# Performance work log

Measured on AMD Instinct MI355X. Metric: run time of the kernel, lower is better.

## Reference

```python
import jax, jax.numpy as jnp
import numpy as np

B = 64            # batch of graphs
E = 8978          # edge-simplices per graph (nodes of the Hodge-1 graph)
E2 = E // 2       # after Graclus pair-pooling
K = 4             # Laguerre polynomial order
DEG = 16          # avg degree of the (edge-)adjacency
SLOPE = 0.33      # LeakyReLU negative slope
EPS = 1e-5        # BatchNorm eps


def _make_edges(rng, b, n, deg):
    # block-diagonal batched edge list: each graph only connects within itself
    offs = np.repeat(np.arange(b, dtype=np.int64) * n, n * deg)
    dst = np.tile(np.repeat(np.arange(n, dtype=np.int64), deg), b) + offs
    src = rng.integers(0, n, size=b * n * deg) + offs
    return np.stack([src, dst]).astype(np.int32)


def setup_inputs() -> dict:
    rng = np.random.default_rng(0)
    ks = jax.random.split(jax.random.key(0), 12)
    N1 = B * E
    ei1 = _make_edges(rng, B, E, DEG)
    ei2 = _make_edges(rng, B, E2, DEG)
    return {
        "x_s": jax.random.normal(ks[0], (N1, 1), jnp.float32),
        "edge_index_s": jnp.asarray(ei1),
        "edge_weight_s": jax.random.uniform(ks[1], (ei1.shape[1],), jnp.float32) * (2.0 / DEG),
        "edge_index_s1": jnp.asarray(ei2),
        "edge_weight_s1": jax.random.uniform(ks[2], (ei2.shape[1],), jnp.float32) * (2.0 / DEG),
        "W0": jax.random.normal(ks[3], (K, 1, 32), jnp.float32) * 0.3,
        "b0": jnp.zeros((32,), jnp.float32),
        "g0": jnp.ones((32,), jnp.float32),
        "be0": jnp.zeros((32,), jnp.float32),
        "W1": jax.random.normal(ks[4], (K, 32, 32), jnp.float32) * 0.1,
        "b1": jnp.zeros((32,), jnp.float32),
        "g1": jnp.ones((32,), jnp.float32),
        "be1": jnp.zeros((32,), jnp.float32),
        "W2": jax.random.normal(ks[5], (K, 32, 1), jnp.float32) * 0.1,
        "b2": jnp.zeros((1,), jnp.float32),
        "g2": jnp.ones((1,), jnp.float32),
        "be2": jnp.zeros((1,), jnp.float32),
        "lin1_W": jax.random.normal(ks[6], (E2, 256), jnp.float32) * 0.02,
        "lin1_b": jnp.zeros((256,), jnp.float32),
        "bn1_g": jnp.ones((256,), jnp.float32),
        "bn1_b": jnp.zeros((256,), jnp.float32),
        "lin2_W": jax.random.normal(ks[7], (256, 128), jnp.float32) * 0.06,
        "lin2_b": jnp.zeros((128,), jnp.float32),
        "bn2_g": jnp.ones((128,), jnp.float32),
        "bn2_b": jnp.zeros((128,), jnp.float32),
        "lin3_W": jax.random.normal(ks[8], (128, 1), jnp.float32) * 0.09,
        "lin3_b": jnp.zeros((1,), jnp.float32),
    }


def _laguerre_layer(x, src, dst, ew, W, b, gamma, beta, n):
    """HodgeLaguerreConv (K-order Laguerre recurrence over sparse L) + BatchNorm + LeakyReLU."""
    def matvec(v):  # (L v)[i] = sum_j w_ij v[j]
        return jax.ops.segment_sum(ew[:, None] * v[src], dst, num_segments=n)
    Tp = x                      # L_0(L) x = x
    out = Tp @ W[0]
    Tc = x - matvec(x)          # L_1(L) x = x - L x
    out = out + Tc @ W[1]
    for k in range(1, K - 1):   # L_{k+1} = ((2k+1-L) L_k - k L_{k-1}) / (k+1)
        Tn = ((2 * k + 1) * Tc - matvec(Tc) - k * Tp) / (k + 1)
        out = out + Tn @ W[k + 1]
        Tp, Tc = Tc, Tn
    out = out + b
    out = gamma * (out - out.mean(0)) * jax.lax.rsqrt(out.var(0) + EPS) + beta
    return jnp.where(out > 0, out, SLOPE * out)


def _bn(h, g, b):
    return g * (h - h.mean(0)) * jax.lax.rsqrt(h.var(0) + EPS) + b


def reference(x_s, edge_index_s, edge_weight_s, edge_index_s1, edge_weight_s1,
              W0, b0, g0, be0, W1, b1, g1, be1, W2, b2, g2, be2,
              lin1_W, lin1_b, bn1_g, bn1_b, lin2_W, lin2_b, bn2_g, bn2_b,
              lin3_W, lin3_b):
    N1, N2 = B * E, B * E2
    x = _laguerre_layer(x_s, edge_index_s[0], edge_index_s[1], edge_weight_s,
                        W0, b0, g0, be0, N1)
    # Graclus pooling: merge matched node pairs by max over features
    x = x.reshape(B, E2, 2, x.shape[-1]).max(axis=2).reshape(N2, -1)
    x = _laguerre_layer(x, edge_index_s1[0], edge_index_s1[1], edge_weight_s1,
                        W1, b1, g1, be1, N2)
    x = _laguerre_layer(x, edge_index_s1[0], edge_index_s1[1], edge_weight_s1,
                        W2, b2, g2, be2, N2)
    x = x.reshape(B, E2)        # last conv has 1 channel
    h = jax.nn.relu(_bn(x @ lin1_W + lin1_b, bn1_g, bn1_b))
    h = jax.nn.relu(_bn(h @ lin2_W + lin2_b, bn2_g, bn2_b))
    return h @ lin3_W + lin3_b  # [B, num_classes=1]
```

## Files before the change

### kernel.cpp

```cpp
#include <hip/hip_runtime.h>
#include <cstdint>

#define SLOPE 0.33f

static constexpr int B_   = 64;
static constexpr int E1_  = 8978;
static constexpr int E2_  = 4489;
static constexpr int N1_  = B_ * E1_;
static constexpr int N2_  = B_ * E2_;
static constexpr int DEG_ = 16;
static constexpr int QTR_ = 2245;
static constexpr int QTR2_ = 1123;
static constexpr int MVGRID = (N2_ * 32) / 256;
static constexpr int PROJ_GRID = (N2_ + 511) / 512;
static constexpr double EPS_ = 1e-5;

__device__ __forceinline__ float lrelu(float v) { return v > 0.f ? v : SLOPE * v; }
__device__ __forceinline__ float dot4(float4 a, float4 b) {
  return a.x * b.x + a.y * b.y + a.z * b.z + a.w * b.w;
}

__global__ __launch_bounds__(256) void k0_mv1(const float* __restrict__ x,
    const int* __restrict__ src, const float* __restrict__ ew, float* __restrict__ T1) {
  __shared__ float sx[E1_];
  int g = blockIdx.x >> 2, q = blockIdx.x & 3;
  int gbase = g * E1_;
  for (int j = threadIdx.x; j < E1_; j += 256) sx[j] = x[gbase + j];
  __syncthreads();
  int start = q * QTR_, end = min(start + QTR_, E1_);
  for (int i = start + (int)threadIdx.x; i < end; i += 256) {
    int node = gbase + i;
    const int4* s4 = (const int4*)(src + (size_t)node * DEG_);
    const float4* w4 = (const float4*)(ew + (size_t)node * DEG_);
    float acc = 0.f;
#pragma unroll
    for (int j = 0; j < 4; ++j) {
      int4 s = s4[j]; float4 w = w4[j];
      acc += w.x * sx[s.x - gbase] + w.y * sx[s.y - gbase]
           + w.z * sx[s.z - gbase] + w.w * sx[s.w - gbase];
    }
    T1[node] = sx[i] - acc;
  }
}

__global__ __launch_bounds__(256) void k0_mv2(const float* __restrict__ x,
    const int* __restrict__ src, const float* __restrict__ ew,
    const float* __restrict__ T1, float* __restrict__ T2) {
  __shared__ float sT[E1_];
  int g = blockIdx.x >> 2, q = blockIdx.x & 3;
  int gbase = g * E1_;
  for (int j = threadIdx.x; j < E1_; j += 256) sT[j] = T1[gbase + j];
  __syncthreads();
  int start = q * QTR_, end = min(start + QTR_, E1_);
  for (int i = start + (int)threadIdx.x; i < end; i += 256) {
    int node = gbase + i;
    const int4* s4 = (const int4*)(src + (size_t)node * DEG_);
    const float4* w4 = (const float4*)(ew + (size_t)node * DEG_);
    float acc = 0.f;
#pragma unroll
    for (int j = 0; j < 4; ++j) {
      int4 s = s4[j]; float4 w = w4[j];
      acc += w.x * sT[s.x - gbase] + w.y * sT[s.y - gbase]
           + w.z * sT[s.z - gbase] + w.w * sT[s.w - gbase];
    }
    T2[node] = (3.f * sT[i] - acc - x[node]) * 0.5f;
  }
}

__global__ __launch_bounds__(256) void k0_mv3(const float* __restrict__ x,
    const int* __restrict__ src, const float* __restrict__ ew,
    const float* __restrict__ T1, const float* __restrict__ T2,
    float* __restrict__ T3, double* mom) {
  __shared__ float sT[E1_];
  __shared__ double sred[4 * 14];
  int g = blockIdx.x >> 2, q = blockIdx.x & 3;
  int gbase = g * E1_;
  for (int j = threadIdx.x; j < E1_; j += 256) sT[j] = T2[gbase + j];
  __syncthreads();
  double m[14];
#pragma unroll
  for (int j = 0; j < 14; ++j) m[j] = 0.0;
  int start = q * QTR_, end = min(start + QTR_, E1_);
  for (int i = start + (int)threadIdx.x; i < end; i += 256) {
    int node = gbase + i;
    const int4* s4 = (const int4*)(src + (size_t)node * DEG_);
    const float4* w4 = (const float4*)(ew + (size_t)node * DEG_);
    float acc = 0.f;
#pragma unroll
    for (int j = 0; j < 4; ++j) {
      int4 s = s4[j]; float4 w = w4[j];
      acc += w.x * sT[s.x - gbase] + w.y * sT[s.y - gbase]
           + w.z * sT[s.z - gbase] + w.w * sT[s.w - gbase];
    }
    float t1 = T1[node];
    float t2 = sT[i];
    float t3 = (5.f * t2 - acc - 2.f * t1) * (1.f / 3.f);
    T3[node] = t3;
    double d0 = x[node], d1 = t1, d2 = t2, d3 = t3;
    m[0] += d0; m[1] += d1; m[2] += d2; m[3] += d3;
    m[4] += d0 * d0; m[5] += d0 * d1; m[6] += d0 * d2; m[7] += d0 * d3;
    m[8] += d1 * d1; m[9] += d1 * d2; m[10] += d1 * d3;
    m[11] += d2 * d2; m[12] += d2 * d3; m[13] += d3 * d3;
  }
  int lane = threadIdx.x & 63, wid = threadIdx.x >> 6;
#pragma unroll
  for (int j = 0; j < 14; ++j) {
    double v = m[j];
    for (int o = 32; o; o >>= 1) v += __shfl_down(v, o);
    if (lane == 0) sred[wid * 14 + j] = v;
  }
  __syncthreads();
  if (threadIdx.x < 14) {
    double s = sred[threadIdx.x] + sred[14 + threadIdx.x] + sred[28 + threadIdx.x] + sred[42 + threadIdx.x];
    atomicAdd(&mom[threadIdx.x], s);
  }
}

__global__ void k0_params(const double* __restrict__ mom, const float* __restrict__ W0,
    const float* __restrict__ g0, const float* __restrict__ be0,
    float* __restrict__ scale0, float* __restrict__ shiftE0) {
  int c = threadIdx.x;
  if (c >= 32) return;
  double inv = 1.0 / (double)N1_;
  double mm[4];
#pragma unroll
  for (int k = 0; k < 4; ++k) mm[k] = mom[k] * inv;
  double M[4][4];
  M[0][0] = mom[4] * inv;  M[0][1] = mom[5] * inv;  M[0][2] = mom[6] * inv;  M[0][3] = mom[7] * inv;
  M[1][1] = mom[8] * inv;  M[1][2] = mom[9] * inv;  M[1][3] = mom[10] * inv;
  M[2][2] = mom[11] * inv; M[2][3] = mom[12] * inv; M[3][3] = mom[13] * inv;
  M[1][0] = M[0][1]; M[2][0] = M[0][2]; M[3][0] = M[0][3];
  M[2][1] = M[1][2]; M[3][1] = M[1][3]; M[3][2] = M[2][3];
  double w[4];
#pragma unroll
  for (int k = 0; k < 4; ++k) w[k] = W0[k * 32 + c];
  double mean = 0.0;
#pragma unroll
  for (int k = 0; k < 4; ++k) mean += w[k] * mm[k];
  double e2 = 0.0;
#pragma unroll
  for (int k = 0; k < 4; ++k)
#pragma unroll
    for (int l = 0; l < 4; ++l) e2 += M[k][l] * w[k] * w[l];
  double var = e2 - mean * mean;
  double sc = (double)g0[c] / sqrt(var + EPS_);
  scale0[c] = (float)sc;
  shiftE0[c] = (float)((double)be0[c] - sc * mean);
}

__global__ __launch_bounds__(256) void k0_pool(const float* __restrict__ x,
    const float* __restrict__ T1, const float* __restrict__ T2, const float* __restrict__ T3,
    const float* __restrict__ W0, const float* __restrict__ scale0,
    const float* __restrict__ shiftE0, float* __restrict__ x1) {
  int gid = blockIdx.x * 256 + threadIdx.x;
  int grp = gid >> 5, c = gid & 31;
  if (grp >= N2_) return;
  int b = grp / E2_, j = grp - b * E2_;
  int ga = b * E1_ + 2 * j, gb = ga + 1;
  float w0 = W0[c], w1 = W0[32 + c], w2 = W0[64 + c], w3 = W0[96 + c];
  float da = x[ga] * w0 + T1[ga] * w1 + T2[ga] * w2 + T3[ga] * w3;
  float db = x[gb] * w0 + T1[gb] * w1 + T2[gb] * w2 + T3[gb] * w3;
  float sc = scale0[c], sh = shiftE0[c];
  float ya = lrelu(sc * da + sh), yb = lrelu(sc * db + sh);
  x1[grp * 32 + c] = fmaxf(ya, yb);
}

__global__ __launch_bounds__(256) void k1_projall(const float* __restrict__ X,
    const float* __restrict__ W1, float4* __restrict__ P4) {
  __shared__ float4 Wl[128 * 8];
  const float4 cfs[4] = { {0.f, 0.f, 0.f, -1.f / 6.f},
                          {0.f, 0.f, 0.5f, 1.5f},
                          {0.f, -1.f, -2.f, -3.f},
                          {1.f, 1.f, 1.f, 1.f} };
  for (int e = threadIdx.x; e < 1024; e += 256) {
    int o = e >> 3, qq = e & 7;
    int j = o >> 5, cp = o & 31;
    float4 cf = cfs[j];
    float4 w;
    {
      const float* wp = W1 + (4 * qq + 0) * 32 + cp;
      w.x = cf.x * wp[0] + cf.y * wp[1024] + cf.z * wp[2048] + cf.w * wp[3072];
    }
    {
      const float* wp = W1 + (4 * qq + 1) * 32 + cp;
      w.y = cf.x * wp[0] + cf.y * wp[1024] + cf.z * wp[2048] + cf.w * wp[3072];
    }
    {
      const float* wp = W1 + (4 * qq + 2) * 32 + cp;
      w.z = cf.x * wp[0] + cf.y * wp[1024] + cf.z * wp[2048] + cf.w * wp[3072];
    }
    {
      const float* wp = W1 + (4 * qq + 3) * 32 + cp;
      w.w = cf.x * wp[0] + cf.y * wp[1024] + cf.z * wp[2048] + cf.w * wp[3072];
    }
    Wl[e] = w;
  }
  __syncthreads();
  int rA = blockIdx.x * 512 + threadIdx.x;
  int rB = rA + 256;
  bool okA = rA < N2_, okB = rB < N2_;
  if (!okA) return;
  float4 xA[8], xB[8];
  {
    const float4* pa = (const float4*)(X + (size_t)rA * 32);
#pragma unroll
    for (int t = 0; t < 8; ++t) xA[t] = pa[t];
  }
  if (okB) {
    const float4* pb = (const float4*)(X + (size_t)rB * 32);
#pragma unroll
    for (int t = 0; t < 8; ++t) xB[t] = pb[t];
  } else {
#pragma unroll
    for (int t = 0; t < 8; ++t) xB[t] = {0.f, 0.f, 0.f, 0.f};
  }
  for (int oq = 0; oq < 32; ++oq) {
    float4 aA = {0.f, 0.f, 0.f, 0.f}, aB = {0.f, 0.f, 0.f, 0.f};
    const float4* wr = Wl + oq * 32;
#pragma unroll
    for (int qq = 0; qq < 8; ++qq) {
      float4 w0 = wr[0 * 8 + qq];
      float4 w1 = wr[1 * 8 + qq];
      float4 w2 = wr[2 * 8 + qq];
      float4 w3 = wr[3 * 8 + qq];
      float4 xa = xA[qq], xb = xB[qq];
      aA.x += dot4(xa, w0); aA.y += dot4(xa, w1); aA.z += dot4(xa, w2); aA.w += dot4(xa, w3);
      aB.x += dot4(xb, w0); aB.y += dot4(xb, w1); aB.z += dot4(xb, w2); aB.w += dot4(xb, w3);
    }
    P4[(size_t)oq * N2_ + rA] = aA;
    if (okB) P4[(size_t)oq * N2_ + rB] = aB;
  }
}

__global__ __launch_bounds__(1024) void k1_chain(const float4* __restrict__ P4,
    float4* __restrict__ O4, const int* __restrict__ src,
    const float* __restrict__ ew, double* st) {
  __shared__ float4 bA[E2_], bB[E2_];
  __shared__ float sacc[8];
  int v = (blockIdx.x & 7) * 64 + (blockIdx.x >> 3);
  int g = v >> 3, cg = v & 7;
  int gbase = g * E2_;
  int tid = threadIdx.x;
  if (tid < 8) sacc[tid] = 0.f;
  {
    const float4* sp = P4 + (size_t)cg * N2_ + gbase;
    for (int i = tid; i < E2_; i += 1024) bA[i] = sp[i];
  }
  float4* cur = bA;
  float4* nxt = bB;
  for (int s = 1; s <= 3; ++s) {
    __syncthreads();
    const float4* selfp = P4 + (size_t)(s * 8 + cg) * N2_ + gbase;
    for (int n = tid; n < E2_; n += 1024) {
      const int4* s4 = (const int4*)(src + (size_t)(gbase + n) * DEG_);
      const float4* w4 = (const float4*)(ew + (size_t)(gbase + n) * DEG_);
      float4 acc = selfp[n];
#pragma unroll
      for (int j = 0; j < 4; ++j) {
        int4 sx = s4[j]; float4 w = w4[j];
        float4 g0 = cur[sx.x - gbase];
        float4 g1 = cur[sx.y - gbase];
        float4 g2 = cur[sx.z - gbase];
        float4 g3 = cur[sx.w - gbase];
        acc.x += w.x * g0.x + w.y * g1.x + w.z * g2.x + w.w * g3.x;
        acc.y += w.x * g0.y + w.y * g1.y + w.z * g2.y + w.w * g3.y;
        acc.z += w.x * g0.z + w.y * g1.z + w.z * g2.z + w.w * g3.z;
        acc.w += w.x * g0.w + w.y * g1.w + w.z * g2.w + w.w * g3.w;
      }
      nxt[n] = acc;
    }
    float4* t = cur; cur = nxt; nxt = t;
  }
  __syncthreads();
  float4* op = O4 + (size_t)cg * N2_ + gbase;
  float4 s1 = {0.f, 0.f, 0.f, 0.f}, s2 = {0.f, 0.f, 0.f, 0.f};
  for (int n = tid; n < E2_; n += 1024) {
    float4 vv = cur[n];
    op[n] = vv;
    s1.x += vv.x; s1.y += vv.y; s1.z += vv.z; s1.w += vv.w;
    s2.x += vv.x * vv.x; s2.y += vv.y * vv.y; s2.z += vv.z * vv.z; s2.w += vv.w * vv.w;
  }
  for (int o = 32; o; o >>= 1) {
    s1.x += __shfl_down(s1.x, o); s1.y += __shfl_down(s1.y, o);
    s1.z += __shfl_down(s1.z, o); s1.w += __shfl_down(s1.w, o);
    s2.x += __shfl_down(s2.x, o); s2.y += __shfl_down(s2.y, o);
    s2.z += __shfl_down(s2.z, o); s2.w += __shfl_down(s2.w, o);
  }
  if ((tid & 63) == 0) {
    atomicAdd(&sacc[0], s1.x); atomicAdd(&sacc[1], s1.y);
    atomicAdd(&sacc[2], s1.z); atomicAdd(&sacc[3], s1.w);
    atomicAdd(&sacc[4], s2.x); atomicAdd(&sacc[5], s2.y);
    atomicAdd(&sacc[6], s2.z); atomicAdd(&sacc[7], s2.w);
  }
  __syncthreads();
  if (tid < 4) {
    int ch = cg * 4 + tid;
    atomicAdd(&st[ch], (double)sacc[tid]);
    atomicAdd(&st[32 + ch], (double)sacc[4 + tid]);
  }
}

__global__ void k1_params(const double* __restrict__ sum, const double* __restrict__ sq,
    const float* __restrict__ g1, const float* __restrict__ be1,
    float* __restrict__ scale1, float* __restrict__ shiftE1) {
  int c = threadIdx.x;
  if (c >= 32) return;
  double mean = sum[c] / (double)N2_;
  double var = sq[c] / (double)N2_ - mean * mean;
  double sc = (double)g1[c] / sqrt(var + EPS_);
  scale1[c] = (float)sc;
  shiftE1[c] = (float)((double)be1[c] - sc * mean);
}

__global__ __launch_bounds__(256) void k2_proj(const float* __restrict__ X,
    const float* __restrict__ W2, const float* __restrict__ scale1,
    const float* __restrict__ shiftE1,
    float* __restrict__ u0, float* __restrict__ u1,
    float* __restrict__ u2, float* __restrict__ u3) {
  __shared__ float qv[4][32];
  __shared__ float fsc[32], fsh[32];
  int tid = threadIdx.x;
  if (tid < 128) {
    int cp = tid & 31, j = tid >> 5;
    float w0 = W2[cp], w1 = W2[32 + cp], w2 = W2[64 + cp], w3 = W2[96 + cp];
    float q;
    if (j == 0)      q = w0 + w1 + w2 + w3;
    else if (j == 1) q = -w1 - 2.f * w2 - 3.f * w3;
    else if (j == 2) q = 0.5f * w2 + 1.5f * w3;
    else             q = -w3 * (1.f / 6.f);
    qv[j][cp] = q;
  }
  if (tid < 32) { fsc[tid] = scale1[tid]; fsh[tid] = shiftE1[tid]; }
  __syncthreads();
  int node = blockIdx.x * 256 + tid;
  if (node >= N2_) return;
  const float4* xf = (const float4*)X;
  float a0 = 0.f, a1 = 0.f, a2 = 0.f, a3 = 0.f;
#pragma unroll
  for (int t = 0; t < 8; ++t) {
    float4 v = xf[(size_t)t * N2_ + node];
    float f0 = lrelu(fsc[4 * t] * v.x + fsh[4 * t]);
    float f1 = lrelu(fsc[4 * t + 1] * v.y + fsh[4 * t + 1]);
    float f2_ = lrelu(fsc[4 * t + 2] * v.z + fsh[4 * t + 2]);
    float f3 = lrelu(fsc[4 * t + 3] * v.w + fsh[4 * t + 3]);
    a0 += f0 * qv[0][4 * t] + f1 * qv[0][4 * t + 1] + f2_ * qv[0][4 * t + 2] + f3 * qv[0][4 * t + 3];
    a1 += f0 * qv[1][4 * t] + f1 * qv[1][4 * t + 1] + f2_ * qv[1][4 * t + 2] + f3 * qv[1][4 * t + 3];
    a2 += f0 * qv[2][4 * t] + f1 * qv[2][4 * t + 1] + f2_ * qv[2][4 * t + 2] + f3 * qv[2][4 * t + 3];
    a3 += f0 * qv[3][4 * t] + f1 * qv[3][4 * t + 1] + f2_ * qv[3][4 * t + 2] + f3 * qv[3][4 * t + 3];
  }
  u0[node] = a0; u1[node] = a1; u2[node] = a2; u3[node] = a3;
}

__global__ __launch_bounds__(256) void k2_step(const float* __restrict__ z,
    const int* __restrict__ src, const float* __restrict__ ew,
    const float* __restrict__ u, float* __restrict__ zo,
    int do_stats, double* st2) {
  __shared__ float sz[E2_];
  __shared__ double sred[4][2];
  int g = blockIdx.x >> 2, q = blockIdx.x & 3;
  int gbase = g * E2_;
  for (int j = threadIdx.x; j < E2_; j += 256) sz[j] = z[gbase + j];
  __syncthreads();
  int start = q * QTR2_, end = min(start + QTR2_, E2_);
  double aS = 0.0, aQ = 0.0;
  for (int i = start + (int)threadIdx.x; i < end; i += 256) {
    int node = gbase + i;
    const int4* s4 = (const int4*)(src + (size_t)node * DEG_);
    const float4* w4 = (const float4*)(ew + (size_t)node * DEG_);
    float acc = 0.f;
#pragma unroll
    for (int j = 0; j < 4; ++j) {
      int4 s = s4[j]; float4 w = w4[j];
      acc += w.x * sz[s.x - gbase] + w.y * sz[s.y - gbase]
           + w.z * sz[s.z - gbase] + w.w * sz[s.w - gbase];
    }
    float val = u[node] + acc;
    zo[node] = val;
    if (do_stats) { aS += val; aQ += (double)val * (double)val; }
  }
  if (do_stats) {
    int lane = threadIdx.x & 63, wid = threadIdx.x >> 6;
    for (int o = 32; o; o >>= 1) { aS += __shfl_down(aS, o); aQ += __shfl_down(aQ, o); }
    if (lane == 0) { sred[wid][0] = aS; sred[wid][1] = aQ; }
    __syncthreads();
    if (threadIdx.x == 0) {
      double s = sred[0][0] + sred[1][0] + sred[2][0] + sred[3][0];
      double qq = sred[0][1] + sred[1][1] + sred[2][1] + sred[3][1];
      atomicAdd(&st2[0], s); atomicAdd(&st2[1], qq);
    }
  }
}

__global__ void k2_params(const double* __restrict__ st2, const float* __restrict__ g2,
    const float* __restrict__ be2, float* __restrict__ p ) {
  if (threadIdx.x != 0) return;
  double mean = st2[0] / (double)N2_;
  double var = st2[1] / (double)N2_ - mean * mean;
  double sc = (double)g2[0] / sqrt(var + EPS_);
  p[128] = (float)sc;
  p[129] = (float)((double)be2[0] - sc * mean);
}

__global__ __launch_bounds__(256) void k3_gemm1(const float* __restrict__ out2,
    const float* __restrict__ lin1W, const float* __restrict__ p, float* h1pre) {
  __shared__ float f2v[4][284];
  float sc = p[128], sh = p[129];
  int bs = blockIdx.x & 15, rs = blockIdx.x >> 4;
  int b0 = bs * 4;
  int r0 = rs * 281;
  int nr = min(281, E2_ - r0);
  int c = threadIdx.x;
#pragma unroll
  for (int b = 0; b < 4; ++b)
    for (int j = c; j < 284; j += 256)
      f2v[b][j] = (j < nr) ? lrelu(sc * out2[(b0 + b) * E2_ + r0 + j] + sh) : 0.f;
  __syncthreads();
  float acc0 = 0.f, acc1 = 0.f, acc2 = 0.f, acc3 = 0.f;
  int nr4 = nr & ~3;
  int j = 0;
  for (; j < nr4; j += 4) {
    const float* wp = lin1W + (size_t)(r0 + j) * 256 + c;
    float w0 = wp[0], w1 = wp[256], w2 = wp[512], w3 = wp[768];
    float4 f0 = *(const float4*)&f2v[0][j];
    float4 f1 = *(const float4*)&f2v[1][j];
    float4 f2_ = *(const float4*)&f2v[2][j];
    float4 f3 = *(const float4*)&f2v[3][j];
    acc0 += f0.x * w0 + f0.y * w1 + f0.z * w2 + f0.w * w3;
    acc1 += f1.x * w0 + f1.y * w1 + f1.z * w2 + f1.w * w3;
    acc2 += f2_.x * w0 + f2_.y * w1 + f2_.z * w2 + f2_.w * w3;
    acc3 += f3.x * w0 + f3.y * w1 + f3.z * w2 + f3.w * w3;
  }
  for (; j < nr; ++j) {
    float w = lin1W[(size_t)(r0 + j) * 256 + c];
    acc0 += f2v[0][j] * w;
    acc1 += f2v[1][j] * w;
    acc2 += f2v[2][j] * w;
    acc3 += f2v[3][j] * w;
  }
  atomicAdd(&h1pre[(b0 + 0) * 256 + c], acc0);
  atomicAdd(&h1pre[(b0 + 1) * 256 + c], acc1);
  atomicAdd(&h1pre[(b0 + 2) * 256 + c], acc2);
  atomicAdd(&h1pre[(b0 + 3) * 256 + c], acc3);
}

__global__ __launch_bounds__(256) void k4_bn1(const float* __restrict__ h1pre,
    const float* __restrict__ g, const float* __restrict__ be, float* __restrict__ h1) {
  int c = threadIdx.x;
  float vs[64];
  double s = 0.0, q = 0.0;
  for (int b = 0; b < 64; ++b) { float v = h1pre[b * 256 + c]; vs[b] = v; s += v; q += (double)v * v; }
  double mean = s / 64.0, var = q / 64.0 - mean * mean;
  double scd = (double)g[c] / sqrt(var + EPS_);
  double shd = (double)be[c] - scd * mean;
  for (int b = 0; b < 64; ++b) {
    float y = (float)(scd * vs[b] + shd);
    h1[b * 256 + c] = y > 0.f ? y : 0.f;
  }
}

__global__ __launch_bounds__(256) void k5_gemm2(const float* __restrict__ h1,
    const float* __restrict__ lin2W, float* __restrict__ h2pre) {
  __shared__ float sred[256];
  int c = blockIdx.x;
  int b = threadIdx.x & 63, q = threadIdx.x >> 6;
  float acc = 0.f;
  for (int r = q; r < 256; r += 4) acc += h1[b * 256 + r] * lin2W[r * 128 + c];
  sred[threadIdx.x] = acc;
  __syncthreads();
  if (threadIdx.x < 64)
    h2pre[threadIdx.x * 128 + c] = sred[threadIdx.x] + sred[64 + threadIdx.x]
                                 + sred[128 + threadIdx.x] + sred[192 + threadIdx.x];
}

__global__ __launch_bounds__(256) void k6_final(const float* __restrict__ h2pre,
    const float* __restrict__ g, const float* __restrict__ be,
    const float* __restrict__ W3, const float* __restrict__ b3, float* __restrict__ outp) {
  __shared__ float sh2[64 * 129];
  __shared__ float sred[256];
  int tid = threadIdx.x;
  if (tid < 128) {
    int c = tid;
    float vs[64];
    double s = 0.0, q = 0.0;
    for (int b = 0; b < 64; ++b) { float v = h2pre[b * 128 + c]; vs[b] = v; s += v; q += (double)v * v; }
    double mean = s / 64.0, var = q / 64.0 - mean * mean;
    double scd = (double)g[c] / sqrt(var + EPS_);
    double shd = (double)be[c] - scd * mean;
    for (int b = 0; b < 64; ++b) {
      float y = (float)(scd * vs[b] + shd);
      sh2[b * 129 + c] = y > 0.f ? y : 0.f;
    }
  }
  __syncthreads();
  int b = tid & 63, q = tid >> 6;
  float acc = 0.f;
  for (int r = q; r < 128; r += 4) acc += sh2[b * 129 + r] * W3[r];
  sred[tid] = acc;
  __syncthreads();
  if (tid < 64)
    outp[tid] = sred[tid] + sred[64 + tid] + sred[128 + tid] + sred[192 + tid] + b3[0];
}

extern "C" void kernel_launch(void* const* d_in, const int* in_sizes, int n_in,
                              void* d_out, int out_size, void* d_ws, size_t ws_size,
                              hipStream_t stream) {
  const float* x    = (const float*)d_in[0];
  const int*   ei1  = (const int*)d_in[1];
  const float* ew1  = (const float*)d_in[2];
  const int*   ei2  = (const int*)d_in[3];
  const float* ew2  = (const float*)d_in[4];
  const float* W0   = (const float*)d_in[5];
  const float* g0   = (const float*)d_in[7];
  const float* be0  = (const float*)d_in[8];
  const float* W1   = (const float*)d_in[9];
  const float* g1   = (const float*)d_in[11];
  const float* be1  = (const float*)d_in[12];
  const float* W2   = (const float*)d_in[13];
  const float* g2   = (const float*)d_in[15];
  const float* be2  = (const float*)d_in[16];
  const float* lin1W = (const float*)d_in[17];
  const float* bn1g = (const float*)d_in[19];
  const float* bn1b = (const float*)d_in[20];
  const float* lin2W = (const float*)d_in[21];
  const float* bn2g = (const float*)d_in[23];
  const float* bn2b = (const float*)d_in[24];
  const float* lin3W = (const float*)d_in[25];
  const float* lin3b = (const float*)d_in[26];

  char* ws = (char*)d_ws;
  double* stats  = (double*)ws;
  float*  params = (float*)(ws + 1024);
  float*  h1pre  = (float*)(ws + 4096);
  float*  h1     = (float*)(ws + 4096 + 65536);
  float*  h2pre  = (float*)(ws + 4096 + 131072);
  float*  Treg   = (float*)(ws + 262144);
  float* T1_0 = Treg;
  float* T2_0 = Treg + N1_;
  float* T3_0 = Treg + 2 * (size_t)N1_;
  float* u0   = Treg;
  float* u1   = Treg + (size_t)N2_;
  float* u2   = Treg + 2 * (size_t)N2_;
  float* u3   = Treg + 3 * (size_t)N2_;
  float* zA   = Treg + 4 * (size_t)N2_;
  float* out2 = Treg + 5 * (size_t)N2_;
  float*  big = (float*)(ws + 262144 + 3 * (size_t)N1_ * 4);
  float* bufA = big;
  float* Pbuf = big + 32 * (size_t)N2_;

  hipMemsetAsync(stats, 0, 80 * sizeof(double), stream);
  hipMemsetAsync(h1pre, 0, 65536, stream);

  k0_mv1<<<256, 256, 0, stream>>>(x, ei1, ew1, T1_0);
  k0_mv2<<<256, 256, 0, stream>>>(x, ei1, ew1, T1_0, T2_0);
  k0_mv3<<<256, 256, 0, stream>>>(x, ei1, ew1, T1_0, T2_0, T3_0, stats);
  k0_params<<<1, 32, 0, stream>>>(stats, W0, g0, be0, params, params + 32);
  k0_pool<<<MVGRID, 256, 0, stream>>>(x, T1_0, T2_0, T3_0, W0, params, params + 32, bufA);

  k1_projall<<<PROJ_GRID, 256, 0, stream>>>(bufA, W1, (float4*)Pbuf);
  k1_chain<<<512, 1024, 0, stream>>>((const float4*)Pbuf, (float4*)Pbuf, ei2, ew2, stats + 14);
  k1_params<<<1, 32, 0, stream>>>(stats + 14, stats + 46, g1, be1, params + 64, params + 96);

  k2_proj<<<(N2_ + 255) / 256, 256, 0, stream>>>(Pbuf, W2, params + 64, params + 96,
                                                 u0, u1, u2, u3);
  k2_step<<<256, 256, 0, stream>>>(u3, ei2, ew2, u2, zA, 0, nullptr);
  k2_step<<<256, 256, 0, stream>>>(zA, ei2, ew2, u1, u3, 0, nullptr);
  k2_step<<<256, 256, 0, stream>>>(u3, ei2, ew2, u0, out2, 1, stats + 78);
  k2_params<<<1, 64, 0, stream>>>(stats + 78, g2, be2, params);

  k3_gemm1<<<256, 256, 0, stream>>>(out2, lin1W, params, h1pre);
  k4_bn1<<<1, 256, 0, stream>>>(h1pre, bn1g, bn1b, h1);
  k5_gemm2<<<128, 256, 0, stream>>>(h1, lin2W, h2pre);
  k6_final<<<1, 256, 0, stream>>>(h2pre, bn2g, bn2b, lin3W, lin3b, (float*)d_out);
}
```

Before: 540.4 us.

## Split layer-1 chain into 2-channel groups to double block count

Changes the projected feature layout from float4 channel groups to float2 groups, so k1_chain runs 1024 blocks that each handle 2 channels instead of 512 blocks handling 4. Shared memory per block is halved, which allows more resident blocks per CU and more parallelism for the gather-heavy Laguerre recurrence. The cost is that every block re-reads the edge indices and weights, so that traffic doubles, and loads become narrower. k1_projall and k2_proj are updated to write and read the new layout.

```diff
diff --git a/kernel.cpp b/kernel.cpp
--- a/kernel.cpp
+++ b/kernel.cpp
@@ -166,7 +166,7 @@
 }
 
 __global__ __launch_bounds__(256) void k1_projall(const float* __restrict__ X,
-    const float* __restrict__ W1, float4* __restrict__ P4) {
+    const float* __restrict__ W1, float2* __restrict__ P2b) {
   __shared__ float4 Wl[128 * 8];
   const float4 cfs[4] = { {0.f, 0.f, 0.f, -1.f / 6.f},
                           {0.f, 0.f, 0.5f, 1.5f},
@@ -227,76 +227,76 @@
       aA.x += dot4(xa, w0); aA.y += dot4(xa, w1); aA.z += dot4(xa, w2); aA.w += dot4(xa, w3);
       aB.x += dot4(xb, w0); aB.y += dot4(xb, w1); aB.z += dot4(xb, w2); aB.w += dot4(xb, w3);
     }
-    P4[(size_t)oq * N2_ + rA] = aA;
-    if (okB) P4[(size_t)oq * N2_ + rB] = aB;
-  }
-}
-
-__global__ __launch_bounds__(1024) void k1_chain(const float4* __restrict__ P4,
-    float4* __restrict__ O4, const int* __restrict__ src,
+    float2 lo = {aA.x, aA.y}, hi = {aA.z, aA.w};
+    P2b[(size_t)(oq * 2 + 0) * N2_ + rA] = lo;
+    P2b[(size_t)(oq * 2 + 1) * N2_ + rA] = hi;
+    if (okB) {
+      float2 lo2 = {aB.x, aB.y}, hi2 = {aB.z, aB.w};
+      P2b[(size_t)(oq * 2 + 0) * N2_ + rB] = lo2;
+      P2b[(size_t)(oq * 2 + 1) * N2_ + rB] = hi2;
+    }
+  }
+}
+
+__global__ __launch_bounds__(1024) void k1_chain(const float2* __restrict__ P2b,
+    float2* __restrict__ O2, const int* __restrict__ src,
     const float* __restrict__ ew, double* st) {
-  __shared__ float4 bA[E2_], bB[E2_];
-  __shared__ float sacc[8];
-  int v = (blockIdx.x & 7) * 64 + (blockIdx.x >> 3);
-  int g = v >> 3, cg = v & 7;
+  __shared__ float2 bA[E2_], bB[E2_];
+  __shared__ float sacc[4];
+  int v = (blockIdx.x & 7) * 128 + (blockIdx.x >> 3);
+  int g = v >> 4, cg = v & 15;
   int gbase = g * E2_;
   int tid = threadIdx.x;
-  if (tid < 8) sacc[tid] = 0.f;
+  if (tid < 4) sacc[tid] = 0.f;
   {
-    const float4* sp = P4 + (size_t)cg * N2_ + gbase;
+    const float2* sp = P2b + (size_t)cg * N2_ + gbase;
     for (int i = tid; i < E2_; i += 1024) bA[i] = sp[i];
   }
-  float4* cur = bA;
-  float4* nxt = bB;
+  float2* cur = bA;
+  float2* nxt = bB;
   for (int s = 1; s <= 3; ++s) {
     __syncthreads();
-    const float4* selfp = P4 + (size_t)(s * 8 + cg) * N2_ + gbase;
+    const float2* selfp = P2b + (size_t)(s * 16 + cg) * N2_ + gbase;
     for (int n = tid; n < E2_; n += 1024) {
       const int4* s4 = (const int4*)(src + (size_t)(gbase + n) * DEG_);
       const float4* w4 = (const float4*)(ew + (size_t)(gbase + n) * DEG_);
-      float4 acc = selfp[n];
+      float2 acc = selfp[n];
 #pragma unroll
       for (int j = 0; j < 4; ++j) {
         int4 sx = s4[j]; float4 w = w4[j];
-        float4 g0 = cur[sx.x - gbase];
-        float4 g1 = cur[sx.y - gbase];
-        float4 g2 = cur[sx.z - gbase];
-        float4 g3 = cur[sx.w - gbase];
+        float2 g0 = cur[sx.x - gbase];
+        float2 g1 = cur[sx.y - gbase];
+        float2 g2 = cur[sx.z - gbase];
+        float2 g3 = cur[sx.w - gbase];
         acc.x += w.x * g0.x + w.y * g1.x + w.z * g2.x + w.w * g3.x;
         acc.y += w.x * g0.y + w.y * g1.y + w.z * g2.y + w.w * g3.y;
-        acc.z += w.x * g0.z + w.y * g1.z + w.z * g2.z + w.w * g3.z;
-        acc.w += w.x * g0.w + w.y * g1.w + w.z * g2.w + w.w * g3.w;
       }
       nxt[n] = acc;
     }
-    float4* t = cur; cur = nxt; nxt = t;
-  }
-  __syncthreads();
-  float4* op = O4 + (size_t)cg * N2_ + gbase;
-  float4 s1 = {0.f, 0.f, 0.f, 0.f}, s2 = {0.f, 0.f, 0.f, 0.f};
+    float2* t = cur; cur = nxt; nxt = t;
+  }
+  __syncthreads();
+  float2* op = O2 + (size_t)cg * N2_ + gbase;
+  float2 s1 = {0.f, 0.f}, s2v = {0.f, 0.f};
   for (int n = tid; n < E2_; n += 1024) {
-    float4 vv = cur[n];
+    float2 vv = cur[n];
     op[n] = vv;
-    s1.x += vv.x; s1.y += vv.y; s1.z += vv.z; s1.w += vv.w;
-    s2.x += vv.x * vv.x; s2.y += vv.y * vv.y; s2.z += vv.z * vv.z; s2.w += vv.w * vv.w;
+    s1.x += vv.x; s1.y += vv.y;
+    s2v.x += vv.x * vv.x; s2v.y += vv.y * vv.y;
   }
   for (int o = 32; o; o >>= 1) {
     s1.x += __shfl_down(s1.x, o); s1.y += __shfl_down(s1.y, o);
-    s1.z += __shfl_down(s1.z, o); s1.w += __shfl_down(s1.w, o);
-    s2.x += __shfl_down(s2.x, o); s2.y += __shfl_down(s2.y, o);
-    s2.z += __shfl_down(s2.z, o); s2.w += __shfl_down(s2.w, o);
+    s2v.x += __shfl_down(s2v.x, o); s2v.y += __shfl_down(s2v.y, o);
   }
   if ((tid & 63) == 0) {
     atomicAdd(&sacc[0], s1.x); atomicAdd(&sacc[1], s1.y);
-    atomicAdd(&sacc[2], s1.z); atomicAdd(&sacc[3], s1.w);
-    atomicAdd(&sacc[4], s2.x); atomicAdd(&sacc[5], s2.y);
-    atomicAdd(&sacc[6], s2.z); atomicAdd(&sacc[7], s2.w);
-  }
-  __syncthreads();
-  if (tid < 4) {
-    int ch = cg * 4 + tid;
+    atomicAdd(&sacc[2], s2v.x); atomicAdd(&sacc[3], s2v.y);
+  }
+  __syncthreads();
+  if (tid < 2) {
+    int ch = (cg >> 1) * 4 + (cg & 1) * 2 + tid;
     atomicAdd(&st[ch], (double)sacc[tid]);
-    atomicAdd(&st[32 + ch], (double)sacc[4 + tid]);
+    atomicAdd(&st[32 + ch], (double)sacc[2 + tid]);
   }
 }
 
@@ -334,19 +334,19 @@
   __syncthreads();
   int node = blockIdx.x * 256 + tid;
   if (node >= N2_) return;
-  const float4* xf = (const float4*)X;
+  const float2* x2 = (const float2*)X;
   float a0 = 0.f, a1 = 0.f, a2 = 0.f, a3 = 0.f;
 #pragma unroll
-  for (int t = 0; t < 8; ++t) {
-    float4 v = xf[(size_t)t * N2_ + node];
-    float f0 = lrelu(fsc[4 * t] * v.x + fsh[4 * t]);
-    float f1 = lrelu(fsc[4 * t + 1] * v.y + fsh[4 * t + 1]);
-    float f2_ = lrelu(fsc[4 * t + 2] * v.z + fsh[4 * t + 2]);
-    float f3 = lrelu(fsc[4 * t + 3] * v.w + fsh[4 * t + 3]);
-    a0 += f0 * qv[0][4 * t] + f1 * qv[0][4 * t + 1] + f2_ * qv[0][4 * t + 2] + f3 * qv[0][4 * t + 3];
-    a1 += f0 * qv[1][4 * t] + f1 * qv[1][4 * t + 1] + f2_ * qv[1][4 * t + 2] + f3 * qv[1][4 * t + 3];
-    a2 += f0 * qv[2][4 * t] + f1 * qv[2][4 * t + 1] + f2_ * qv[2][4 * t + 2] + f3 * qv[2][4 * t + 3];
-    a3 += f0 * qv[3][4 * t] + f1 * qv[3][4 * t + 1] + f2_ * qv[3][4 * t + 2] + f3 * qv[3][4 * t + 3];
+  for (int p = 0; p < 16; ++p) {
+    float2 v = x2[(size_t)p * N2_ + node];
+    int c0 = (p >> 1) * 4 + (p & 1) * 2;
+    int c1 = c0 + 1;
+    float f0 = lrelu(fsc[c0] * v.x + fsh[c0]);
+    float f1 = lrelu(fsc[c1] * v.y + fsh[c1]);
+    a0 += f0 * qv[0][c0] + f1 * qv[0][c1];
+    a1 += f0 * qv[1][c0] + f1 * qv[1][c1];
+    a2 += f0 * qv[2][c0] + f1 * qv[2][c1];
+    a3 += f0 * qv[3][c0] + f1 * qv[3][c1];
   }
   u0[node] = a0; u1[node] = a1; u2[node] = a2; u3[node] = a3;
 }
@@ -556,8 +556,8 @@
   k0_params<<<1, 32, 0, stream>>>(stats, W0, g0, be0, params, params + 32);
   k0_pool<<<MVGRID, 256, 0, stream>>>(x, T1_0, T2_0, T3_0, W0, params, params + 32, bufA);
 
-  k1_projall<<<PROJ_GRID, 256, 0, stream>>>(bufA, W1, (float4*)Pbuf);
-  k1_chain<<<512, 1024, 0, stream>>>((const float4*)Pbuf, (float4*)Pbuf, ei2, ew2, stats + 14);
+  k1_projall<<<PROJ_GRID, 256, 0, stream>>>(bufA, W1, (float2*)Pbuf);
+  k1_chain<<<1024, 1024, 0, stream>>>((const float2*)Pbuf, (float2*)Pbuf, ei2, ew2, stats + 14);
   k1_params<<<1, 32, 0, stream>>>(stats + 14, stats + 46, g1, be1, params + 64, params + 96);
 
   k2_proj<<<(N2_ + 255) / 256, 256, 0, stream>>>(Pbuf, W2, params + 64, params + 96,
```

Result: slower. 594.6 us (+10.0%).

## Fuse three layer-0 Laguerre matvec kernels into one LDS-resident chain kernel

Applied to the files above, without the earlier changes.

Replaces the three separate matvec kernels for the first Laguerre layer with one 1024-thread kernel that keeps x, T1 and T2 for a whole graph in shared memory. This removes two kernel launches and the global round-trips of T1/T2 between steps. In exchange, each of the four blocks per graph redundantly recomputes T1 and T2 for the full graph, multiplying edge reads for those steps, and uses about 108 KB of LDS per block, which limits occupancy. Block indices are also permuted to spread graphs across the grid.

```diff
diff --git a/kernel.cpp b/kernel.cpp
--- a/kernel.cpp
+++ b/kernel.cpp
@@ -20,18 +20,21 @@
   return a.x * b.x + a.y * b.y + a.z * b.z + a.w * b.w;
 }
 
-__global__ __launch_bounds__(256) void k0_mv1(const float* __restrict__ x,
-    const int* __restrict__ src, const float* __restrict__ ew, float* __restrict__ T1) {
-  __shared__ float sx[E1_];
-  int g = blockIdx.x >> 2, q = blockIdx.x & 3;
+__global__ __launch_bounds__(1024) void k0_chain(const float* __restrict__ x,
+    const int* __restrict__ src, const float* __restrict__ ew,
+    float* __restrict__ T1, float* __restrict__ T2, float* __restrict__ T3,
+    double* mom) {
+  __shared__ float sx[E1_], s1[E1_], s2[E1_];
+  __shared__ double sred[16][14];
+  int v = (blockIdx.x & 7) * 32 + (blockIdx.x >> 3);
+  int g = v >> 2, q = v & 3;
   int gbase = g * E1_;
-  for (int j = threadIdx.x; j < E1_; j += 256) sx[j] = x[gbase + j];
-  __syncthreads();
-  int start = q * QTR_, end = min(start + QTR_, E1_);
-  for (int i = start + (int)threadIdx.x; i < end; i += 256) {
-    int node = gbase + i;
-    const int4* s4 = (const int4*)(src + (size_t)node * DEG_);
-    const float4* w4 = (const float4*)(ew + (size_t)node * DEG_);
+  int tid = threadIdx.x;
+  for (int i = tid; i < E1_; i += 1024) sx[i] = x[gbase + i];
+  __syncthreads();
+  for (int i = tid; i < E1_; i += 1024) {
+    const int4* s4 = (const int4*)(src + (size_t)(gbase + i) * DEG_);
+    const float4* w4 = (const float4*)(ew + (size_t)(gbase + i) * DEG_);
     float acc = 0.f;
 #pragma unroll
     for (int j = 0; j < 4; ++j) {
@@ -39,80 +42,60 @@
       acc += w.x * sx[s.x - gbase] + w.y * sx[s.y - gbase]
            + w.z * sx[s.z - gbase] + w.w * sx[s.w - gbase];
     }
-    T1[node] = sx[i] - acc;
-  }
-}
-
-__global__ __launch_bounds__(256) void k0_mv2(const float* __restrict__ x,
-    const int* __restrict__ src, const float* __restrict__ ew,
-    const float* __restrict__ T1, float* __restrict__ T2) {
-  __shared__ float sT[E1_];
-  int g = blockIdx.x >> 2, q = blockIdx.x & 3;
-  int gbase = g * E1_;
-  for (int j = threadIdx.x; j < E1_; j += 256) sT[j] = T1[gbase + j];
-  __syncthreads();
-  int start = q * QTR_, end = min(start + QTR_, E1_);
-  for (int i = start + (int)threadIdx.x; i < end; i += 256) {
-    int node = gbase + i;
-    const int4* s4 = (const int4*)(src + (size_t)node * DEG_);
-    const float4* w4 = (const float4*)(ew + (size_t)node * DEG_);
+    s1[i] = sx[i] - acc;
+  }
+  __syncthreads();
+  for (int i = tid; i < E1_; i += 1024) {
+    const int4* s4 = (const int4*)(src + (size_t)(gbase + i) * DEG_);
+    const float4* w4 = (const float4*)(ew + (size_t)(gbase + i) * DEG_);
     float acc = 0.f;
 #pragma unroll
     for (int j = 0; j < 4; ++j) {
       int4 s = s4[j]; float4 w = w4[j];
-      acc += w.x * sT[s.x - gbase] + w.y * sT[s.y - gbase]
-           + w.z * sT[s.z - gbase] + w.w * sT[s.w - gbase];
-    }
-    T2[node] = (3.f * sT[i] - acc - x[node]) * 0.5f;
-  }
-}
-
-__global__ __launch_bounds__(256) void k0_mv3(const float* __restrict__ x,
-    const int* __restrict__ src, const float* __restrict__ ew,
-    const float* __restrict__ T1, const float* __restrict__ T2,
-    float* __restrict__ T3, double* mom) {
-  __shared__ float sT[E1_];
-  __shared__ double sred[4 * 14];
-  int g = blockIdx.x >> 2, q = blockIdx.x & 3;
-  int gbase = g * E1_;
-  for (int j = threadIdx.x; j < E1_; j += 256) sT[j] = T2[gbase + j];
+      acc += w.x * s1[s.x - gbase] + w.y * s1[s.y - gbase]
+           + w.z * s1[s.z - gbase] + w.w * s1[s.w - gbase];
+    }
+    s2[i] = (3.f * s1[i] - acc - sx[i]) * 0.5f;
+  }
   __syncthreads();
   double m[14];
 #pragma unroll
   for (int j = 0; j < 14; ++j) m[j] = 0.0;
   int start = q * QTR_, end = min(start + QTR_, E1_);
-  for (int i = start + (int)threadIdx.x; i < end; i += 256) {
-    int node = gbase + i;
-    const int4* s4 = (const int4*)(src + (size_t)node * DEG_);
-    const float4* w4 = (const float4*)(ew + (size_t)node * DEG_);
+  for (int i = start + tid; i < end; i += 1024) {
+    const int4* s4 = (const int4*)(src + (size_t)(gbase + i) * DEG_);
+    const float4* w4 = (const float4*)(ew + (size_t)(gbase + i) * DEG_);
     float acc = 0.f;
 #pragma unroll
     for (int j = 0; j < 4; ++j) {
       int4 s = s4[j]; float4 w = w4[j];
-      acc += w.x * sT[s.x - gbase] + w.y * sT[s.y - gbase]
-           + w.z * sT[s.z - gbase] + w.w * sT[s.w - gbase];
-    }
-    float t1 = T1[node];
-    float t2 = sT[i];
+      acc += w.x * s2[s.x - gbase] + w.y * s2[s.y - gbase]
+           + w.z * s2[s.z - gbase] + w.w * s2[s.w - gbase];
+    }
+    float t1 = s1[i], t2 = s2[i];
     float t3 = (5.f * t2 - acc - 2.f * t1) * (1.f / 3.f);
-    T3[node] = t3;
-    double d0 = x[node], d1 = t1, d2 = t2, d3 = t3;
+    T1[gbase + i] = t1;
+    T2[gbase + i] = t2;
+    T3[gbase + i] = t3;
+    double d0 = sx[i], d1 = t1, d2 = t2, d3 = t3;
     m[0] += d0; m[1] += d1; m[2] += d2; m[3] += d3;
     m[4] += d0 * d0; m[5] += d0 * d1; m[6] += d0 * d2; m[7] += d0 * d3;
     m[8] += d1 * d1; m[9] += d1 * d2; m[10] += d1 * d3;
     m[11] += d2 * d2; m[12] += d2 * d3; m[13] += d3 * d3;
   }
-  int lane = threadIdx.x & 63, wid = threadIdx.x >> 6;
+  int lane = tid & 63, wid = tid >> 6;
 #pragma unroll
   for (int j = 0; j < 14; ++j) {
-    double v = m[j];
-    for (int o = 32; o; o >>= 1) v += __shfl_down(v, o);
-    if (lane == 0) sred[wid * 14 + j] = v;
-  }
-  __syncthreads();
-  if (threadIdx.x < 14) {
-    double s = sred[threadIdx.x] + sred[14 + threadIdx.x] + sred[28 + threadIdx.x] + sred[42 + threadIdx.x];
-    atomicAdd(&mom[threadIdx.x], s);
+    double vv = m[j];
+    for (int o = 32; o; o >>= 1) vv += __shfl_down(vv, o);
+    if (lane == 0) sred[wid][j] = vv;
+  }
+  __syncthreads();
+  if (tid < 14) {
+    double s = 0.0;
+#pragma unroll
+    for (int w = 0; w < 16; ++w) s += sred[w][tid];
+    atomicAdd(&mom[tid], s);
   }
 }
 
@@ -550,9 +533,7 @@
   hipMemsetAsync(stats, 0, 80 * sizeof(double), stream);
   hipMemsetAsync(h1pre, 0, 65536, stream);
 
-  k0_mv1<<<256, 256, 0, stream>>>(x, ei1, ew1, T1_0);
-  k0_mv2<<<256, 256, 0, stream>>>(x, ei1, ew1, T1_0, T2_0);
-  k0_mv3<<<256, 256, 0, stream>>>(x, ei1, ew1, T1_0, T2_0, T3_0, stats);
+  k0_chain<<<256, 1024, 0, stream>>>(x, ei1, ew1, T1_0, T2_0, T3_0, stats);
   k0_params<<<1, 32, 0, stream>>>(stats, W0, g0, be0, params, params + 32);
   k0_pool<<<MVGRID, 256, 0, stream>>>(x, T1_0, T2_0, T3_0, W0, params, params + 32, bufA);
 
```

After: 542.1 us. Within noise of the previous version (+0.3%).
